# Kernel tuning notes

Hardware: AMD Instinct MI355X
Metric: run time of the kernel (lower is better)

The kernel has to match this reference:

```python
import jax, jax.numpy as jnp
import numpy as np
from jax.scipy.linalg import expm

B, NUM_WS, Z_DIM, MAT_DIM = 4096, 16, 512, 10
INIT_SCALE = 0.001


def setup_inputs() -> dict:
    key = jax.random.key(0)
    k1, k2 = jax.random.split(key)
    z = jax.random.normal(k1, (B, NUM_WS, Z_DIM), dtype=jnp.float32)
    # learned Lie-algebra basis, initialized N(0, init_scale) as in the module
    lie_alg_basis = jax.random.normal(k2, (NUM_WS, Z_DIM, MAT_DIM, MAT_DIM), dtype=jnp.float32) * INIT_SCALE
    return {"z": z, "lie_alg_basis": lie_alg_basis}


def reference(z, lie_alg_basis):
    # weighted sum of basis matrices per (batch, ws): [b, w, m, m]
    lie_alg = jnp.einsum('bwz,wzij->bwij', z, lie_alg_basis)
    b, w, m, _ = lie_alg.shape
    # batched small matrix exponential over b*w tiny (m x m) matrices
    lie_group = jax.vmap(expm)(lie_alg.reshape(b * w, m, m))
    return lie_group.reshape(b, w, m, m)
```

## Files before the change

### kernel.cpp

```cpp
#include <hip/hip_runtime.h>
#include <hip/hip_bf16.h>

#define NWS 16
#define ZD 512
#define MM 100
#define NCOL 112
#define QBYTES 28672
#define PANEL_BYTES 114688

typedef __attribute__((ext_vector_type(8))) short bf16x8;
typedef __attribute__((ext_vector_type(4))) float f32x4;

static __device__ __forceinline__ unsigned short f2bf(float x) {
    union { __hip_bfloat16 h; unsigned short u; } cv;
    cv.h = __float2bfloat16(x);
    return cv.u;
}

__global__ __launch_bounds__(256) void prep_basis(const float* __restrict__ basis,
                                                  unsigned char* __restrict__ Bt) {
    const int idx = blockIdx.x * 256 + threadIdx.x;
    const int col  = idx % NCOL;
    const int rest = idx / NCOL;
    const int g    = rest & 63;
    const int w    = rest >> 6;

    bf16x8 pk;
    #pragma unroll
    for (int e = 0; e < 8; ++e) {
        const int k = g * 8 + e;
        const float v = (col < MM) ? basis[((size_t)(w * ZD + k)) * MM + col] : 0.f;
        pk[e] = (short)f2bf(v);
    }
    const int q  = g >> 4;
    const int gl = g & 15;
    const size_t off = (size_t)w * PANEL_BYTES + (size_t)q * QBYTES
                     + (size_t)col * 256 + (size_t)((gl * 16) ^ ((col & 7) << 4));
    *reinterpret_cast<bf16x8*>(Bt + off) = pk;
}

__global__ __launch_bounds__(512, 4) void einsum_mfma(const float* __restrict__ z,
                                                      const unsigned char* __restrict__ Btg,
                                                      float* __restrict__ out) {
    __shared__ __align__(16) unsigned char Bs[2][QBYTES];
    const int w     = blockIdx.x;
    const int chunk = blockIdx.y;
    const int tid   = threadIdx.x;
    const int wave  = tid >> 6;
    const int lane  = tid & 63;
    const int l15   = lane & 15;
    const int k8    = lane >> 4;

    const int row = chunk * 128 + wave * 16 + l15;
    const float* zp = z + (size_t)row * (NWS * ZD) + (size_t)w * ZD + k8 * 8;
    const unsigned char* bt = Btg + (size_t)w * PANEL_BYTES;

    int bbase[7];
    #pragma unroll
    for (int nf = 0; nf < 7; ++nf) bbase[nf] = (nf * 16 + l15) * 256;
    const int bswz = (l15 & 7) << 4;

    float4 zf[8];

    #define STAGE_Q(t, buf)                                                              \
        do {                                                                             \
            const unsigned char* gq = bt + (t) * QBYTES;                                 \
            _Pragma("unroll")                                                            \
            for (int r = 0; r < 3; ++r) {                                                \
                __builtin_amdgcn_global_load_lds(                                        \
                    (const __attribute__((address_space(1))) unsigned int*)(gq + (r * 512 + tid) * 16), \
                    (__attribute__((address_space(3))) unsigned int*)(&Bs[buf][(r * 512 + tid) * 16]),  \
                    16, 0, 0);                                                           \
            }                                                                            \
            if (tid < 256) {                                                             \
                __builtin_amdgcn_global_load_lds(                                        \
                    (const __attribute__((address_space(1))) unsigned int*)(gq + (1536 + tid) * 16),    \
                    (__attribute__((address_space(3))) unsigned int*)(&Bs[buf][(1536 + tid) * 16]),     \
                    16, 0, 0);                                                           \
            }                                                                            \
        } while (0)

    #define ZLOAD_Q(t)                                                                   \
        do {                                                                             \
            _Pragma("unroll")                                                            \
            for (int j = 0; j < 4; ++j) {                                                \
                zf[2 * j]     = *reinterpret_cast<const float4*>(zp + ((t) * 4 + j) * 32);      \
                zf[2 * j + 1] = *reinterpret_cast<const float4*>(zp + ((t) * 4 + j) * 32 + 4);  \
            }                                                                            \
        } while (0)

    f32x4 acc[7];
    #pragma unroll
    for (int nf = 0; nf < 7; ++nf) acc[nf] = (f32x4){0.f, 0.f, 0.f, 0.f};

    STAGE_Q(0, 0);
    ZLOAD_Q(0);
    __syncthreads();

    #pragma unroll
    for (int t = 0; t < 4; ++t) {
        bf16x8 zb[4];
        #pragma unroll
        for (int j = 0; j < 4; ++j) {
            zb[j][0] = (short)f2bf(zf[2 * j].x);
            zb[j][1] = (short)f2bf(zf[2 * j].y);
            zb[j][2] = (short)f2bf(zf[2 * j].z);
            zb[j][3] = (short)f2bf(zf[2 * j].w);
            zb[j][4] = (short)f2bf(zf[2 * j + 1].x);
            zb[j][5] = (short)f2bf(zf[2 * j + 1].y);
            zb[j][6] = (short)f2bf(zf[2 * j + 1].z);
            zb[j][7] = (short)f2bf(zf[2 * j + 1].w);
        }
        if (t < 3) {
            STAGE_Q(t + 1, (t + 1) & 1);
            ZLOAD_Q(t + 1);
        }
        #pragma unroll
        for (int s = 0; s < 4; ++s) {
            const int klb = (s * 64 + k8 * 16) ^ bswz;
            #pragma unroll
            for (int nf = 0; nf < 7; ++nf) {
                const bf16x8 bfr = *reinterpret_cast<const bf16x8*>(&Bs[t & 1][bbase[nf] + klb]);
                acc[nf] = __builtin_amdgcn_mfma_f32_16x16x32_bf16(zb[s], bfr, acc[nf], 0, 0, 0);
            }
        }
        if (t < 3) __syncthreads();
    }

    const int rowbase = chunk * 128 + wave * 16 + k8 * 4;
    #pragma unroll
    for (int nf = 0; nf < 7; ++nf) {
        const int col = nf * 16 + l15;
        if (col < MM) {
            #pragma unroll
            for (int r = 0; r < 4; ++r)
                out[((size_t)(rowbase + r) * NWS + w) * MM + col] = acc[nf][r];
        }
    }
    #undef STAGE_Q
    #undef ZLOAD_Q
}

#define EXP_NT 6

__global__ __launch_bounds__(320, 2) void expm_kernel(float* __restrict__ out) {
    __shared__ float As[64 * 100];
    const int t = threadIdx.x;
    const size_t base = (size_t)blockIdx.x * 6400;

    #pragma unroll
    for (int q = 0; q < 5; ++q) {
        const int idx = (q * 320 + t) * 4;
        *reinterpret_cast<float4*>(&As[idx]) =
            *reinterpret_cast<const float4*>(out + base + idx);
    }
    __syncthreads();

    const int m  = t / 5;
    const int c  = t - m * 5;
    const int j0 = 2 * c, j1 = j0 + 1;
    const float* A = &As[m * 100];

    float a[100];
    #pragma unroll
    for (int q = 0; q < 25; ++q) {
        const float4 v = *reinterpret_cast<const float4*>(A + q * 4);
        a[q * 4 + 0] = v.x; a[q * 4 + 1] = v.y;
        a[q * 4 + 2] = v.z; a[q * 4 + 3] = v.w;
    }

    float p0[10], p1[10];
    #pragma unroll
    for (int i = 0; i < 10; ++i) {
        p0[i] = A[i * 10 + j0] * (1.f / EXP_NT) + ((i == j0) ? 1.f : 0.f);
        p1[i] = A[i * 10 + j1] * (1.f / EXP_NT) + ((i == j1) ? 1.f : 0.f);
    }

    #pragma unroll
    for (int k = EXP_NT - 1; k >= 1; --k) {
        float n0[10], n1[10];
        #pragma unroll
        for (int i = 0; i < 10; ++i) { n0[i] = 0.f; n1[i] = 0.f; }
        #pragma unroll
        for (int kk = 0; kk < 10; ++kk) {
            const float q0 = p0[kk], q1 = p1[kk];
            #pragma unroll
            for (int i = 0; i < 10; ++i) {
                n0[i] = fmaf(a[i * 10 + kk], q0, n0[i]);
                n1[i] = fmaf(a[i * 10 + kk], q1, n1[i]);
            }
        }
        const float invk = 1.f / (float)k;
        #pragma unroll
        for (int i = 0; i < 10; ++i) {
            p0[i] = n0[i] * invk + ((i == j0) ? 1.f : 0.f);
            p1[i] = n1[i] * invk + ((i == j1) ? 1.f : 0.f);
        }
    }

    #pragma unroll
    for (int i = 0; i < 10; ++i)
        *reinterpret_cast<float2*>(out + base + m * 100 + i * 10 + j0) =
            make_float2(p0[i], p1[i]);
}

extern "C" void kernel_launch(void* const* d_in, const int* in_sizes, int n_in,
                              void* d_out, int out_size, void* d_ws, size_t ws_size,
                              hipStream_t stream) {
    const float* z     = (const float*)d_in[0];
    const float* basis = (const float*)d_in[1];
    float* out = (float*)d_out;
    unsigned char* Bt = (unsigned char*)d_ws;

    prep_basis<<<(NWS * 64 * NCOL) / 256, 256, 0, stream>>>(basis, Bt);

    dim3 gridA(NWS, 32);
    einsum_mfma<<<gridA, 512, 0, stream>>>(z, Bt, out);

    expm_kernel<<<(4096 * NWS) / 64, 320, 0, stream>>>(out);
}
```

Measured before the change: 58.34 us.

## Shrink einsum tiles to 64 rows and 8 K-stages with half-size LDS buffers

The einsum kernel now uses 256-thread blocks covering 64 rows instead of 512 threads covering 128. The K loop is split into 8 stages of 64 instead of 4 stages of 128, and the basis panel layout is rebuilt to match, halving the LDS double buffer. The grid is swapped so chunks vary fastest and blocks for the same w share the basis panel in cache. This gives more blocks and less LDS per block, which should raise occupancy and overlap. The costs are twice as many barriers and twice the total basis traffic from L2 into LDS.

```diff
diff --git a/kernel.cpp b/kernel.cpp
--- a/kernel.cpp
+++ b/kernel.cpp
@@ -5,8 +5,9 @@
 #define ZD 512
 #define MM 100
 #define NCOL 112
-#define QBYTES 28672
+#define EBYTES 14336
 #define PANEL_BYTES 114688
+#define EXP_NT 6
 
 typedef __attribute__((ext_vector_type(8))) short bf16x8;
 typedef __attribute__((ext_vector_type(4))) float f32x4;
@@ -32,60 +33,60 @@
         const float v = (col < MM) ? basis[((size_t)(w * ZD + k)) * MM + col] : 0.f;
         pk[e] = (short)f2bf(v);
     }
-    const int q  = g >> 4;
-    const int gl = g & 15;
-    const size_t off = (size_t)w * PANEL_BYTES + (size_t)q * QBYTES
-                     + (size_t)col * 256 + (size_t)((gl * 16) ^ ((col & 7) << 4));
+    const int e8  = g >> 3;
+    const int gl8 = g & 7;
+    const size_t off = (size_t)w * PANEL_BYTES + (size_t)e8 * EBYTES
+                     + (size_t)col * 128 + (size_t)((gl8 * 16) ^ ((col & 7) << 4));
     *reinterpret_cast<bf16x8*>(Bt + off) = pk;
 }
 
-__global__ __launch_bounds__(512, 4) void einsum_mfma(const float* __restrict__ z,
+__global__ __launch_bounds__(256, 4) void einsum_mfma(const float* __restrict__ z,
                                                       const unsigned char* __restrict__ Btg,
                                                       float* __restrict__ out) {
-    __shared__ __align__(16) unsigned char Bs[2][QBYTES];
-    const int w     = blockIdx.x;
-    const int chunk = blockIdx.y;
+    __shared__ __align__(16) unsigned char Bs[2][EBYTES];
+    const int chunk = blockIdx.x;
+    const int w     = blockIdx.y;
     const int tid   = threadIdx.x;
     const int wave  = tid >> 6;
     const int lane  = tid & 63;
     const int l15   = lane & 15;
     const int k8    = lane >> 4;
 
-    const int row = chunk * 128 + wave * 16 + l15;
+    const int row = chunk * 64 + wave * 16 + l15;
     const float* zp = z + (size_t)row * (NWS * ZD) + (size_t)w * ZD + k8 * 8;
     const unsigned char* bt = Btg + (size_t)w * PANEL_BYTES;
 
     int bbase[7];
     #pragma unroll
-    for (int nf = 0; nf < 7; ++nf) bbase[nf] = (nf * 16 + l15) * 256;
+    for (int nf = 0; nf < 7; ++nf) bbase[nf] = (nf * 16 + l15) * 128;
     const int bswz = (l15 & 7) << 4;
 
-    float4 zf[8];
-
-    #define STAGE_Q(t, buf)                                                              \
+    float4 zf[4];
+
+    #define STAGE_E(t, buf)                                                              \
         do {                                                                             \
-            const unsigned char* gq = bt + (t) * QBYTES;                                 \
+            const unsigned char* gq = bt + (t) * EBYTES;                                 \
             _Pragma("unroll")                                                            \
             for (int r = 0; r < 3; ++r) {                                                \
                 __builtin_amdgcn_global_load_lds(                                        \
-                    (const __attribute__((address_space(1))) unsigned int*)(gq + (r * 512 + tid) * 16), \
-                    (__attribute__((address_space(3))) unsigned int*)(&Bs[buf][(r * 512 + tid) * 16]),  \
+                    (const __attribute__((address_space(1))) unsigned int*)(gq + (r * 256 + tid) * 16), \
+                    (__attribute__((address_space(3))) unsigned int*)(&Bs[buf][(r * 256 + tid) * 16]),  \
                     16, 0, 0);                                                           \
             }                                                                            \
-            if (tid < 256) {                                                             \
+            if (tid < 128) {                                                             \
                 __builtin_amdgcn_global_load_lds(                                        \
-                    (const __attribute__((address_space(1))) unsigned int*)(gq + (1536 + tid) * 16),    \
-                    (__attribute__((address_space(3))) unsigned int*)(&Bs[buf][(1536 + tid) * 16]),     \
+                    (const __attribute__((address_space(1))) unsigned int*)(gq + (768 + tid) * 16),     \
+                    (__attribute__((address_space(3))) unsigned int*)(&Bs[buf][(768 + tid) * 16]),      \
                     16, 0, 0);                                                           \
             }                                                                            \
         } while (0)
 
-    #define ZLOAD_Q(t)                                                                   \
+    #define ZLOAD_E(t)                                                                   \
         do {                                                                             \
             _Pragma("unroll")                                                            \
-            for (int j = 0; j < 4; ++j) {                                                \
-                zf[2 * j]     = *reinterpret_cast<const float4*>(zp + ((t) * 4 + j) * 32);      \
-                zf[2 * j + 1] = *reinterpret_cast<const float4*>(zp + ((t) * 4 + j) * 32 + 4);  \
+            for (int j = 0; j < 2; ++j) {                                                \
+                zf[2 * j]     = *reinterpret_cast<const float4*>(zp + ((t) * 2 + j) * 32);      \
+                zf[2 * j + 1] = *reinterpret_cast<const float4*>(zp + ((t) * 2 + j) * 32 + 4);  \
             }                                                                            \
         } while (0)
 
@@ -93,15 +94,15 @@
     #pragma unroll
     for (int nf = 0; nf < 7; ++nf) acc[nf] = (f32x4){0.f, 0.f, 0.f, 0.f};
 
-    STAGE_Q(0, 0);
-    ZLOAD_Q(0);
+    STAGE_E(0, 0);
+    ZLOAD_E(0);
     __syncthreads();
 
     #pragma unroll
-    for (int t = 0; t < 4; ++t) {
-        bf16x8 zb[4];
-        #pragma unroll
-        for (int j = 0; j < 4; ++j) {
+    for (int t = 0; t < 8; ++t) {
+        bf16x8 zb[2];
+        #pragma unroll
+        for (int j = 0; j < 2; ++j) {
             zb[j][0] = (short)f2bf(zf[2 * j].x);
             zb[j][1] = (short)f2bf(zf[2 * j].y);
             zb[j][2] = (short)f2bf(zf[2 * j].z);
@@ -111,12 +112,12 @@
             zb[j][6] = (short)f2bf(zf[2 * j + 1].z);
             zb[j][7] = (short)f2bf(zf[2 * j + 1].w);
         }
-        if (t < 3) {
-            STAGE_Q(t + 1, (t + 1) & 1);
-            ZLOAD_Q(t + 1);
-        }
-        #pragma unroll
-        for (int s = 0; s < 4; ++s) {
+        if (t < 7) {
+            STAGE_E(t + 1, (t + 1) & 1);
+            ZLOAD_E(t + 1);
+        }
+        #pragma unroll
+        for (int s = 0; s < 2; ++s) {
             const int klb = (s * 64 + k8 * 16) ^ bswz;
             #pragma unroll
             for (int nf = 0; nf < 7; ++nf) {
@@ -124,10 +125,12 @@
                 acc[nf] = __builtin_amdgcn_mfma_f32_16x16x32_bf16(zb[s], bfr, acc[nf], 0, 0, 0);
             }
         }
-        if (t < 3) __syncthreads();
-    }
-
-    const int rowbase = chunk * 128 + wave * 16 + k8 * 4;
+        if (t < 7) __syncthreads();
+    }
+    #undef STAGE_E
+    #undef ZLOAD_E
+
+    const int rowbase = chunk * 64 + wave * 16 + k8 * 4;
     #pragma unroll
     for (int nf = 0; nf < 7; ++nf) {
         const int col = nf * 16 + l15;
@@ -137,11 +140,7 @@
                 out[((size_t)(rowbase + r) * NWS + w) * MM + col] = acc[nf][r];
         }
     }
-    #undef STAGE_Q
-    #undef ZLOAD_Q
-}
-
-#define EXP_NT 6
+}
 
 __global__ __launch_bounds__(320, 2) void expm_kernel(float* __restrict__ out) {
     __shared__ float As[64 * 100];
@@ -214,8 +213,8 @@
 
     prep_basis<<<(NWS * 64 * NCOL) / 256, 256, 0, stream>>>(basis, Bt);
 
-    dim3 gridA(NWS, 32);
-    einsum_mfma<<<gridA, 512, 0, stream>>>(z, Bt, out);
+    dim3 gridA(64, NWS);
+    einsum_mfma<<<gridA, 256, 0, stream>>>(z, Bt, out);
 
     expm_kernel<<<(4096 * NWS) / 64, 320, 0, stream>>>(out);
 }
```

Result: faster. 57.09 us (-2.1%).
